# Performance work log

Hardware: AMD Instinct MI355X
Metric: run time of the kernel (lower is better)

## Reference

```python
import jax, jax.numpy as jnp
import numpy as np

IN_F = 2048
OUT_F = 2048
BS = 64  # block_size
NIB = IN_F // BS   # 32 in-blocks
NOB = OUT_F // BS  # 32 out-blocks


def setup_inputs() -> dict:
    key = jax.random.key(0)
    k_x, k_s1, k_s2, k_m = jax.random.split(key, 4)
    bound = 1.0 / np.sqrt(BS)
    x = jax.random.normal(k_x, (4, 4096, IN_F), dtype=jnp.float32)
    stage1 = jax.random.uniform(k_s1, (NIB * BS, BS), minval=-bound, maxval=bound, dtype=jnp.float32)
    stage2 = jax.random.uniform(k_s2, (NOB * BS, BS), minval=-bound, maxval=bound, dtype=jnp.float32)
    mix_w = jax.random.normal(k_m, (NOB * BS, NIB * BS), dtype=jnp.float32) / np.sqrt(IN_F)
    return {"x": x, "stage1": stage1, "stage2": stage2, "mix_w": mix_w}


def _blockdiag(x, weight, num_blocks):
    # x: [..., num_blocks*BS]; weight: [num_blocks*BS, BS] viewed as [g, c, d]
    shape = x.shape[:-1]
    xg = x.reshape(-1, num_blocks, BS)
    w = weight.reshape(num_blocks, BS, BS)
    y = jnp.einsum('ngc,gcd->ngd', xg, w)
    return y.reshape(*shape, num_blocks * BS)


def _shuffle(x):
    # interpret last dim as [BS, NIB], transpose to [NIB, BS]
    shape = x.shape[:-1]
    return x.reshape(-1, BS, NIB).transpose(0, 2, 1).reshape(*shape, NIB * BS)


def reference(x, stage1, stage2, mix_w):
    h = _blockdiag(x, stage1, NIB)          # [B,S,IN_F]
    h = _shuffle(h)                          # [B,S,IN_F]
    h = jnp.einsum('bsi,oi->bso', h, mix_w)  # dense mix, no bias
    return _blockdiag(h, stage2, NOB)        # [B,S,OUT_F]
```

## Files before the change

### kernel.cpp

```cpp
#include <hip/hip_runtime.h>
#include <stdint.h>

#define IN_F 2048
#define OUT_F 2048
#define MTOK 16384

typedef __attribute__((ext_vector_type(8))) __bf16 bf16x8;
typedef __attribute__((ext_vector_type(4))) float f32x4;
typedef __attribute__((ext_vector_type(4))) unsigned short us4;

typedef const __attribute__((address_space(1))) void g_void;
typedef __attribute__((address_space(3))) void l_void;

__device__ __forceinline__ void async16(void* lds, const void* g) {
    __builtin_amdgcn_global_load_lds((g_void*)(uintptr_t)g, (l_void*)(uintptr_t)lds, 16, 0, 0);
}

__device__ __forceinline__ unsigned short f2bf(float x) {
    union { float f; uint32_t u; } v; v.f = x;
    uint32_t r = v.u + 0x7fffu + ((v.u >> 16) & 1u);
    return (unsigned short)(r >> 16);
}

__global__ __launch_bounds__(256) void k_convert(
    const float* __restrict__ X, unsigned short* __restrict__ Xb) {
    const int gid = blockIdx.x * 256 + threadIdx.x;
    const float4* src = (const float4*)X;
    us4* dst = (us4*)Xb;
#pragma unroll
    for (int k = 0; k < 16; ++k) {
        int idx = k * (2048 * 256) + gid;
        float4 v = src[idx];
        us4 o;
        o[0] = f2bf(v.x); o[1] = f2bf(v.y); o[2] = f2bf(v.z); o[3] = f2bf(v.w);
        dst[idx] = o;
    }
}

#define FP 68

__global__ __launch_bounds__(256) void k_fold(
    const float* __restrict__ s1, const float* __restrict__ s2,
    const float* __restrict__ MW, unsigned short* __restrict__ Bb) {
    __shared__ float B0[64 * FP];
    __shared__ float B1[64 * FP];
    const int t = threadIdx.x;
    const int g  = blockIdx.x & 31;
    const int rt = blockIdx.x >> 5;
    const int l = t & 15, h = t >> 4;

#pragma unroll
    for (int q = 0; q < 4; ++q) {
        int id = q * 256 + t;
        int c = id >> 4, d4 = id & 15;
        *(float4*)&B0[c * FP + d4 * 4] =
            *(const float4*)(s1 + (size_t)(g * 64 + c) * 64 + d4 * 4);
    }
#pragma unroll
    for (int q = 0; q < 8; ++q) {
        int id = q * 256 + t;
        int o = id >> 5, b = id & 31;
        float2 v = *(const float2*)(MW + (size_t)(rt * 64 + o) * 2048 + b * 64 + g * 2);
        B1[o * FP + b]      = v.x;
        B1[o * FP + b + 32] = v.y;
    }
    __syncthreads();

    float acc[4][4];
#pragma unroll
    for (int i = 0; i < 4; ++i)
#pragma unroll
        for (int j = 0; j < 4; ++j) acc[i][j] = 0.f;
    {
        const int co = l * 4, oo = h * 4;
#pragma unroll
        for (int dc = 0; dc < 16; ++dc) {
            const int dce = (dc + l) & 15;
            float4 bv[4], wv[4];
#pragma unroll
            for (int i = 0; i < 4; ++i) bv[i] = *(const float4*)&B1[(oo + i) * FP + dce * 4];
#pragma unroll
            for (int j = 0; j < 4; ++j) wv[j] = *(const float4*)&B0[(co + j) * FP + dce * 4];
#pragma unroll
            for (int i = 0; i < 4; ++i)
#pragma unroll
                for (int j = 0; j < 4; ++j)
                    acc[i][j] += bv[i].x * wv[j].x + bv[i].y * wv[j].y
                               + bv[i].z * wv[j].z + bv[i].w * wv[j].w;
        }
    }
    __syncthreads();

    {
        const int co = l * 4, oo = h * 4;
#pragma unroll
        for (int j = 0; j < 4; ++j) {
            float4 v; v.x = acc[0][j]; v.y = acc[1][j]; v.z = acc[2][j]; v.w = acc[3][j];
            *(float4*)&B0[(co + j) * FP + oo] = v;
        }
    }
#pragma unroll
    for (int q = 0; q < 4; ++q) {
        int id = q * 256 + t;
        int c2 = id >> 4, d4 = id & 15;
        *(float4*)&B1[c2 * FP + d4 * 4] =
            *(const float4*)(s2 + (size_t)(rt * 64 + c2) * 64 + d4 * 4);
    }
    __syncthreads();

    {
        const int d2o = l * 4, cco = h * 4;
#pragma unroll
        for (int i = 0; i < 4; ++i)
#pragma unroll
            for (int j = 0; j < 4; ++j) acc[i][j] = 0.f;
#pragma unroll
        for (int kc = 0; kc < 16; ++kc) {
            const int kce = (kc + l) & 15;
            float4 wv4[4], mv[4];
#pragma unroll
            for (int s = 0; s < 4; ++s) wv4[s] = *(const float4*)&B1[(kce * 4 + s) * FP + d2o];
#pragma unroll
            for (int j = 0; j < 4; ++j) mv[j] = *(const float4*)&B0[(cco + j) * FP + kce * 4];
#pragma unroll
            for (int i = 0; i < 4; ++i)
#pragma unroll
                for (int j = 0; j < 4; ++j)
                    acc[i][j] += wv4[0][i] * mv[j].x + wv4[1][i] * mv[j].y
                               + wv4[2][i] * mv[j].z + wv4[3][i] * mv[j].w;
        }
#pragma unroll
        for (int i = 0; i < 4; ++i) {
            us4 o;
            o[0] = f2bf(acc[i][0]); o[1] = f2bf(acc[i][1]);
            o[2] = f2bf(acc[i][2]); o[3] = f2bf(acc[i][3]);
            *(us4*)(Bb + (size_t)(rt * 64 + d2o + i) * 2048 + g * 64 + cco) = o;
        }
    }
}

__global__ __launch_bounds__(256, 2) void k_gemm(
    const unsigned short* __restrict__ A, const unsigned short* __restrict__ B,
    float* __restrict__ C) {
    __shared__ unsigned short smem[16384];
    unsigned short* As = smem;
    unsigned short* Bs = smem + 8192;
    const int t = threadIdx.x;
    const int lane = t & 63, wave = t >> 6;
    const int quad = lane >> 4, l16 = lane & 15;
    const int mw = wave & 1, nw = wave >> 1;
    const int orig = blockIdx.y * 128 + blockIdx.x;
    const int lin = (orig & 7) * 256 + (orig >> 3);
    const int m0 = (lin >> 4) * 128;
    const int n0 = (lin & 15) * 128;
    const int rr = t >> 3, chunk = t & 7;
    const int gsw = (chunk ^ (rr & 7)) * 8;
    const int lsw = l16 & 7;

    f32x4 acc[4][4];
#pragma unroll
    for (int i = 0; i < 4; ++i)
#pragma unroll
        for (int j = 0; j < 4; ++j) acc[i][j] = (f32x4)0.f;

    for (int kb = 0; kb < IN_F; kb += 64) {
#pragma unroll
        for (int q = 0; q < 4; ++q) {
            int r = q * 32 + rr;
            async16((char*)As + (size_t)(q * 4096 + t * 16),
                    A + (size_t)(m0 + r) * IN_F + kb + gsw);
            async16((char*)Bs + (size_t)(q * 4096 + t * 16),
                    B + (size_t)(n0 + r) * IN_F + kb + gsw);
        }
        __syncthreads();
#pragma unroll
        for (int ks = 0; ks < 2; ++ks) {
            bf16x8 af[4], bfr[4];
#pragma unroll
            for (int i = 0; i < 4; ++i)
                af[i] = *(const bf16x8*)(As + (mw * 64 + i * 16 + l16) * 64
                                            + (((ks * 4 + quad) ^ lsw) * 8));
#pragma unroll
            for (int j = 0; j < 4; ++j)
                bfr[j] = *(const bf16x8*)(Bs + (nw * 64 + j * 16 + l16) * 64
                                             + (((ks * 4 + quad) ^ lsw) * 8));
#pragma unroll
            for (int i = 0; i < 4; ++i)
#pragma unroll
                for (int j = 0; j < 4; ++j)
                    acc[i][j] = __builtin_amdgcn_mfma_f32_16x16x32_bf16(af[i], bfr[j], acc[i][j], 0, 0, 0);
        }
        __syncthreads();
    }

#pragma unroll
    for (int i = 0; i < 4; ++i)
#pragma unroll
        for (int j = 0; j < 4; ++j) {
            float* Cp = C + (size_t)(m0 + mw * 64 + i * 16 + quad * 4) * OUT_F
                          + (n0 + nw * 64 + j * 16 + l16);
#pragma unroll
            for (int r = 0; r < 4; ++r) Cp[(size_t)r * OUT_F] = acc[i][j][r];
        }
}

extern "C" void kernel_launch(void* const* d_in, const int* in_sizes, int n_in,
                              void* d_out, int out_size, void* d_ws, size_t ws_size,
                              hipStream_t stream) {
    const float* x  = (const float*)d_in[0];
    const float* s1 = (const float*)d_in[1];
    const float* s2 = (const float*)d_in[2];
    const float* mw = (const float*)d_in[3];
    float* out = (float*)d_out;

    char* ws = (char*)d_ws;
    unsigned short* Xb = (unsigned short*)ws;
    unsigned short* Bb = (unsigned short*)(ws + (size_t)MTOK * IN_F * 2);

    k_fold<<<1024, 256, 0, stream>>>(s1, s2, mw, Bb);
    k_convert<<<2048, 256, 0, stream>>>(x, Xb);
    k_gemm<<<dim3(128, 16), 256, 0, stream>>>(Xb, Bb, out);
}
```

Baseline: 419.0 us.

## Fuse fp32-to-bf16 conversion of X into GEMM A-tile loads; pre-permute mix weights

Removes the separate conversion kernel that wrote a bf16 copy of X. The GEMM now loads fp32 X directly, converts it in registers and stores the swizzled bf16 tile to LDS, which saves a full write and re-read of the activation tensor. A new permutation kernel transposes the mix weights into a layout that lets the fold kernel use coalesced float4 loads instead of strided float2 gathers. The cost is that the GEMM reads twice as many A bytes per tile through synchronous register loads rather than async LDS loads, which can hurt latency hiding in the main loop.

```diff
diff --git a/kernel.cpp b/kernel.cpp
--- a/kernel.cpp
+++ b/kernel.cpp
@@ -8,6 +8,7 @@
 typedef __attribute__((ext_vector_type(8))) __bf16 bf16x8;
 typedef __attribute__((ext_vector_type(4))) float f32x4;
 typedef __attribute__((ext_vector_type(4))) unsigned short us4;
+typedef __attribute__((ext_vector_type(8))) unsigned short us8;
 
 typedef const __attribute__((address_space(1))) void g_void;
 typedef __attribute__((address_space(3))) void l_void;
@@ -22,18 +23,26 @@
     return (unsigned short)(r >> 16);
 }
 
-__global__ __launch_bounds__(256) void k_convert(
-    const float* __restrict__ X, unsigned short* __restrict__ Xb) {
-    const int gid = blockIdx.x * 256 + threadIdx.x;
-    const float4* src = (const float4*)X;
-    us4* dst = (us4*)Xb;
-#pragma unroll
-    for (int k = 0; k < 16; ++k) {
-        int idx = k * (2048 * 256) + gid;
-        float4 v = src[idx];
-        us4 o;
-        o[0] = f2bf(v.x); o[1] = f2bf(v.y); o[2] = f2bf(v.z); o[3] = f2bf(v.w);
-        dst[idx] = o;
+__global__ __launch_bounds__(256) void k_perm(
+    const float* __restrict__ MW, float* __restrict__ Bpf) {
+    __shared__ float buf[2112];
+    const int t = threadIdx.x;
+    const float* src = MW + (size_t)blockIdx.x * 2048;
+    float* dst = Bpf + (size_t)blockIdx.x * 2048;
+#pragma unroll
+    for (int q = 0; q < 2; ++q) {
+        int id4 = q * 256 + t;
+        float4 v = *(const float4*)(src + id4 * 4);
+        int i = id4 * 4;
+        int b = i + (i >> 5);
+        buf[b] = v.x; buf[b + 1] = v.y; buf[b + 2] = v.z; buf[b + 3] = v.w;
+    }
+    __syncthreads();
+#pragma unroll
+    for (int q = 0; q < 8; ++q) {
+        int j = q * 256 + t;
+        int i = ((j & 31) << 6) | (j >> 5);
+        dst[j] = buf[i + (i >> 5)];
     }
 }
 
@@ -41,7 +50,7 @@
 
 __global__ __launch_bounds__(256) void k_fold(
     const float* __restrict__ s1, const float* __restrict__ s2,
-    const float* __restrict__ MW, unsigned short* __restrict__ Bb) {
+    const float* __restrict__ Bpf, unsigned short* __restrict__ Bb) {
     __shared__ float B0[64 * FP];
     __shared__ float B1[64 * FP];
     const int t = threadIdx.x;
@@ -57,12 +66,11 @@
             *(const float4*)(s1 + (size_t)(g * 64 + c) * 64 + d4 * 4);
     }
 #pragma unroll
-    for (int q = 0; q < 8; ++q) {
+    for (int q = 0; q < 4; ++q) {
         int id = q * 256 + t;
-        int o = id >> 5, b = id & 31;
-        float2 v = *(const float2*)(MW + (size_t)(rt * 64 + o) * 2048 + b * 64 + g * 2);
-        B1[o * FP + b]      = v.x;
-        B1[o * FP + b + 32] = v.y;
+        int o = id >> 4, d4 = id & 15;
+        *(float4*)&B1[o * FP + d4 * 4] =
+            *(const float4*)(Bpf + (size_t)(rt * 64 + o) * 2048 + g * 64 + d4 * 4);
     }
     __syncthreads();
 
@@ -140,7 +148,7 @@
 }
 
 __global__ __launch_bounds__(256, 2) void k_gemm(
-    const unsigned short* __restrict__ A, const unsigned short* __restrict__ B,
+    const float* __restrict__ X, const unsigned short* __restrict__ B,
     float* __restrict__ C) {
     __shared__ unsigned short smem[16384];
     unsigned short* As = smem;
@@ -164,13 +172,27 @@
         for (int j = 0; j < 4; ++j) acc[i][j] = (f32x4)0.f;
 
     for (int kb = 0; kb < IN_F; kb += 64) {
+        float4 a0[4], a1[4];
+#pragma unroll
+        for (int q = 0; q < 4; ++q) {
+            const float* xp = X + (size_t)(m0 + q * 32 + rr) * IN_F + kb + chunk * 8;
+            a0[q] = *(const float4*)xp;
+            a1[q] = *(const float4*)(xp + 4);
+        }
 #pragma unroll
         for (int q = 0; q < 4; ++q) {
             int r = q * 32 + rr;
-            async16((char*)As + (size_t)(q * 4096 + t * 16),
-                    A + (size_t)(m0 + r) * IN_F + kb + gsw);
             async16((char*)Bs + (size_t)(q * 4096 + t * 16),
                     B + (size_t)(n0 + r) * IN_F + kb + gsw);
+        }
+#pragma unroll
+        for (int q = 0; q < 4; ++q) {
+            us8 pk;
+            pk[0] = f2bf(a0[q].x); pk[1] = f2bf(a0[q].y);
+            pk[2] = f2bf(a0[q].z); pk[3] = f2bf(a0[q].w);
+            pk[4] = f2bf(a1[q].x); pk[5] = f2bf(a1[q].y);
+            pk[6] = f2bf(a1[q].z); pk[7] = f2bf(a1[q].w);
+            *(us8*)(As + (q * 32 + rr) * 64 + gsw) = pk;
         }
         __syncthreads();
 #pragma unroll
@@ -214,10 +236,10 @@
     float* out = (float*)d_out;
 
     char* ws = (char*)d_ws;
-    unsigned short* Xb = (unsigned short*)ws;
-    unsigned short* Bb = (unsigned short*)(ws + (size_t)MTOK * IN_F * 2);
-
-    k_fold<<<1024, 256, 0, stream>>>(s1, s2, mw, Bb);
-    k_convert<<<2048, 256, 0, stream>>>(x, Xb);
-    k_gemm<<<dim3(128, 16), 256, 0, stream>>>(Xb, Bb, out);
-}
+    float* Bpf = (float*)ws;
+    unsigned short* Bb = (unsigned short*)(ws + ((size_t)16 << 20));
+
+    k_perm<<<2048, 256, 0, stream>>>(mw, Bpf);
+    k_fold<<<1024, 256, 0, stream>>>(s1, s2, Bpf, Bb);
+    k_gemm<<<dim3(128, 16), 256, 0, stream>>>(x, Bb, out);
+}
```

Result: slower. 490.7 us (+17.1%).
